# Kernel tuning notes

Hardware: AMD Instinct MI355X
Metric: run time of the kernel (lower is better)

## Reference

```python
import jax, jax.numpy as jnp
import numpy as np

B, S, D = 8, 1024, 1024

def setup_inputs() -> dict:
    key = jax.random.key(0)
    k1, k2, k3, k4, k5 = jax.random.split(key, 5)
    head = jax.random.normal(k1, (B, S, D), dtype=jnp.float32)
    dep = jax.random.normal(k2, (B, S, D), dtype=jnp.float32)
    edge_U = jax.random.normal(k3, (D, D), dtype=jnp.float32) * (1.0 / np.sqrt(D))
    edge_W = jax.random.normal(k4, (1, 2 * D), dtype=jnp.float32) * (1.0 / np.sqrt(2 * D))
    edge_b = jax.random.normal(k5, (1,), dtype=jnp.float32)
    return {"head": head, "dep": dep, "edge_U": edge_U, "edge_W": edge_W, "edge_b": edge_b}

def reference(head, dep, edge_U, edge_W, edge_b):
    # t1[b,i,j] = head[b,i,:] @ edge_U @ dep[b,j,:]
    t1 = jnp.einsum('bid,dk,bjk->bij', head, edge_U, dep)
    # t2: original concatenates [head_i ; dep_j] for every (i,j) pair and applies
    # edge_W [1, 2D]. Algebraically t2[b,i,j] = head_i @ W[:D] + dep_j @ W[D:],
    # so we compute two [B,S] projections and broadcast-add (same math, no
    # O(B*S^2*2D) intermediate).
    d = head.shape[-1]
    w = edge_W[0]
    s_head = head @ w[:d]   # [B, S]
    s_dep = dep @ w[d:]     # [B, S]
    return t1 + s_head[:, :, None] + s_dep[:, None, :] + edge_b[0]
```

## Files before the change

### kernel.cpp

```cpp
#include <hip/hip_runtime.h>
#include <hip/hip_bf16.h>
#include <stdint.h>

#define D_DIM 1024
#define B_DIM 8
#define S_DIM 1024

typedef __bf16 bf16;
typedef __bf16 bf16x4 __attribute__((ext_vector_type(4)));
typedef __bf16 bf16x8 __attribute__((ext_vector_type(8)));
typedef float floatx4 __attribute__((ext_vector_type(4)));

__device__ __forceinline__ void async_copy16(const void* g, void* l) {
    __builtin_amdgcn_global_load_lds(
        (const __attribute__((address_space(1))) void*)g,
        (__attribute__((address_space(3))) void*)l, 16, 0, 0);
}

__global__ __launch_bounds__(256) void prep_kernel(
    const float* __restrict__ head, const float* __restrict__ dep,
    const float* __restrict__ U, const float* __restrict__ edge_W,
    bf16* __restrict__ head_b, bf16* __restrict__ dep_b,
    bf16* __restrict__ U_b,
    float* __restrict__ s_head, float* __restrict__ s_dep)
{
    int blk  = blockIdx.x;
    int wid  = threadIdx.x >> 6;
    int lane = threadIdx.x & 63;

    if (blk < 4096) {
        int row = blk * 4 + wid;

        const float* src;
        bf16* dst;
        const float* w;
        float* sout;
        if (row < B_DIM * S_DIM) {
            src  = head   + (size_t)row * D_DIM;
            dst  = head_b + (size_t)row * D_DIM;
            w    = edge_W;
            sout = s_head + row;
        } else {
            int r = row - B_DIM * S_DIM;
            src  = dep   + (size_t)r * D_DIM;
            dst  = dep_b + (size_t)r * D_DIM;
            w    = edge_W + D_DIM;
            sout = s_dep + r;
        }
        float d = 0.0f;
        #pragma unroll
        for (int it = 0; it < 4; ++it) {
            int idx = it * 64 + lane;
            float4 v  = ((const float4*)src)[idx];
            float4 wv = ((const float4*)w)[idx];
            bf16x4 o;
            o[0] = (bf16)v.x; o[1] = (bf16)v.y; o[2] = (bf16)v.z; o[3] = (bf16)v.w;
            ((bf16x4*)dst)[idx] = o;
            d += v.x * wv.x + v.y * wv.y + v.z * wv.z + v.w * wv.w;
        }
        #pragma unroll
        for (int off = 32; off > 0; off >>= 1)
            d += __shfl_down(d, off, 64);
        if (lane == 0) *sout = d;
    } else {
        int row = (blk - 4096) * 4 + wid;
        const float* src = U   + (size_t)row * D_DIM;
        bf16*        dst = U_b + (size_t)row * D_DIM;
        #pragma unroll
        for (int it = 0; it < 4; ++it) {
            int idx = it * 64 + lane;
            float4 v = ((const float4*)src)[idx];
            bf16x4 o;
            o[0] = (bf16)v.x; o[1] = (bf16)v.y; o[2] = (bf16)v.z; o[3] = (bf16)v.w;
            ((bf16x4*)dst)[idx] = o;
        }
    }
}

template <int EPI>
__global__ __launch_bounds__(512, 4) void gemm_bt_kernel(
    const bf16* __restrict__ A, const bf16* __restrict__ Bt,
    void* __restrict__ Cout,
    int N,
    long long sA, long long sB, long long sC,
    const float* __restrict__ s_row, const float* __restrict__ s_col,
    const float* __restrict__ bias)
{
    const int BK = 64;
    __shared__ bf16 As[128 * BK];
    __shared__ bf16 Bs[128 * BK];

    int tid  = threadIdx.x;
    int wid  = tid >> 6;
    int lane = tid & 63;
    int quad = lane >> 4;
    int l16  = lane & 15;
    int wr   = wid >> 2;
    int wc   = wid & 3;

    int nx  = gridDim.x, ny = gridDim.y;
    int lin = blockIdx.x + nx * (blockIdx.y + ny * blockIdx.z);
    int nwg = nx * ny * gridDim.z;
    int swz = (lin & 7) * (nwg >> 3) + (lin >> 3);
    int bx  = swz % nx;
    int rem = swz / nx;
    int by  = rem % ny;
    int bz  = rem / ny;

    int tile_m = by * 128;
    int tile_n = bx * 128;

    const bf16* Ab = A  + (size_t)bz * sA + (size_t)tile_m * D_DIM;
    const bf16* Bb = Bt + (size_t)bz * sB + (size_t)tile_n * D_DIM;

    floatx4 zero = {0.0f, 0.0f, 0.0f, 0.0f};
    floatx4 acc[4][2];
    #pragma unroll
    for (int i = 0; i < 4; ++i)
        #pragma unroll
        for (int j = 0; j < 2; ++j) acc[i][j] = zero;

    for (int k0 = 0; k0 < D_DIM; k0 += BK) {
        #pragma unroll
        for (int it = 0; it < 2; ++it) {
            int g  = wid * 128 + it * 64 + lane;
            int r  = g >> 3;
            int cg = (g & 7) ^ (r & 7);
            int ldsoff = (wid * 128 + it * 64) * 8;
            async_copy16(Ab + (size_t)r * D_DIM + k0 + cg * 8, &As[ldsoff]);
            async_copy16(Bb + (size_t)r * D_DIM + k0 + cg * 8, &Bs[ldsoff]);
        }
        __syncthreads();

        #pragma unroll
        for (int kk = 0; kk < BK; kk += 32) {
            bf16x8 a[4], b[2];
            #pragma unroll
            for (int mt = 0; mt < 4; ++mt) {
                int row  = wr * 64 + mt * 16 + l16;
                int slot = ((kk >> 3) + quad) ^ (row & 7);
                a[mt] = *(const bf16x8*)&As[row * BK + slot * 8];
            }
            #pragma unroll
            for (int nt = 0; nt < 2; ++nt) {
                int row  = wc * 32 + nt * 16 + l16;
                int slot = ((kk >> 3) + quad) ^ (row & 7);
                b[nt] = *(const bf16x8*)&Bs[row * BK + slot * 8];
            }
            #pragma unroll
            for (int mt = 0; mt < 4; ++mt)
                #pragma unroll
                for (int nt = 0; nt < 2; ++nt)
                    acc[mt][nt] = __builtin_amdgcn_mfma_f32_16x16x32_bf16(
                        a[mt], b[nt], acc[mt][nt], 0, 0, 0);
        }
        __syncthreads();
    }

    int row0 = tile_m + wr * 64;
    int col0 = tile_n + wc * 32;
    if (EPI == 0) {
        bf16* Cb = (bf16*)Cout + (size_t)bz * sC;
        #pragma unroll
        for (int mt = 0; mt < 4; ++mt)
            #pragma unroll
            for (int r = 0; r < 4; ++r) {
                int row = row0 + mt * 16 + quad * 4 + r;
                #pragma unroll
                for (int nt = 0; nt < 2; ++nt) {
                    int col = col0 + nt * 16 + l16;
                    Cb[(size_t)row * N + col] = (bf16)acc[mt][nt][r];
                }
            }
    } else {
        float* Cf = (float*)Cout + (size_t)bz * sC;
        float b0 = bias[0];
        const float* srow = s_row + (size_t)bz * S_DIM;
        const float* scol = s_col + (size_t)bz * S_DIM;
        #pragma unroll
        for (int mt = 0; mt < 4; ++mt)
            #pragma unroll
            for (int r = 0; r < 4; ++r) {
                int row = row0 + mt * 16 + quad * 4 + r;
                float sh = srow[row] + b0;
                #pragma unroll
                for (int nt = 0; nt < 2; ++nt) {
                    int col = col0 + nt * 16 + l16;
                    __builtin_nontemporal_store(acc[mt][nt][r] + sh + scol[col],
                                                &Cf[(size_t)row * N + col]);
                }
            }
    }
}

extern "C" void kernel_launch(void* const* d_in, const int* in_sizes, int n_in,
                              void* d_out, int out_size, void* d_ws, size_t ws_size,
                              hipStream_t stream) {
    const float* head   = (const float*)d_in[0];
    const float* dep    = (const float*)d_in[1];
    const float* edge_U = (const float*)d_in[2];
    const float* edge_W = (const float*)d_in[3];
    const float* edge_b = (const float*)d_in[4];
    float* out = (float*)d_out;

    char* ws = (char*)d_ws;
    const size_t nBSD = (size_t)B_DIM * S_DIM * D_DIM;

    bf16*  head_b = (bf16*)ws;  ws += nBSD * sizeof(bf16);
    bf16*  dep_b  = (bf16*)ws;  ws += nBSD * sizeof(bf16);
    bf16*  U_b    = (bf16*)ws;  ws += (size_t)D_DIM * D_DIM * sizeof(bf16);
    bf16*  tmpD   = (bf16*)ws;  ws += nBSD * sizeof(bf16);
    float* s_head = (float*)ws; ws += (size_t)B_DIM * S_DIM * sizeof(float);
    float* s_dep  = (float*)ws; ws += (size_t)B_DIM * S_DIM * sizeof(float);

    prep_kernel<<<4096 + 256, 256, 0, stream>>>(
        head, dep, edge_U, edge_W, head_b, dep_b, U_b, s_head, s_dep);

    gemm_bt_kernel<0><<<dim3(D_DIM / 128, (B_DIM * S_DIM) / 128, 1), 512, 0, stream>>>(
        dep_b, U_b, tmpD, D_DIM,
        0, 0, 0, nullptr, nullptr, nullptr);

    gemm_bt_kernel<1><<<dim3(S_DIM / 128, S_DIM / 128, B_DIM), 512, 0, stream>>>(
        head_b, tmpD, out, S_DIM,
        (long long)S_DIM * D_DIM, (long long)S_DIM * D_DIM,
        (long long)S_DIM * S_DIM,
        s_head, s_dep, edge_b);
}
```

Before: 156.5 us.

## Double-buffer LDS K-slabs and enlarge GEMM tile to 256x128

Reworks the bf16 GEMM kernel so it prefetches the next K-slab into a second LDS buffer while MFMAs run on the current one, using explicit vmcnt waits and raw barriers. The M tile grows from 128 to 256, giving each wave 8x2 accumulators for more reuse of the B fragments. MFMA blocks are wrapped in s_setprio. The aim is to hide global-to-LDS latency and cut per-FLOP load traffic. The cost is more LDS and more registers (launch bounds drop to 2 blocks), and half as many workgroups, which lowers occupancy and parallelism across CUs.

```diff
diff --git a/kernel.cpp b/kernel.cpp
--- a/kernel.cpp
+++ b/kernel.cpp
@@ -77,8 +77,29 @@
     }
 }
 
+__device__ __forceinline__ void stage_slab(
+    const bf16* __restrict__ Ab, const bf16* __restrict__ Bb,
+    bf16* As, bf16* Bs, int k0, int wid, int lane)
+{
+    #pragma unroll
+    for (int it = 0; it < 4; ++it) {
+        int g  = wid * 256 + it * 64 + lane;
+        int r  = g >> 3;
+        int cg = (g & 7) ^ (r & 7);
+        int ldsoff = (wid * 256 + it * 64) * 8;
+        async_copy16(Ab + (size_t)r * D_DIM + k0 + cg * 8, &As[ldsoff]);
+        if (it < 2) {
+            int gb  = wid * 128 + it * 64 + lane;
+            int rb  = gb >> 3;
+            int cgb = (gb & 7) ^ (rb & 7);
+            int ldsoffb = (wid * 128 + it * 64) * 8;
+            async_copy16(Bb + (size_t)rb * D_DIM + k0 + cgb * 8, &Bs[ldsoffb]);
+        }
+    }
+}
+
 template <int EPI>
-__global__ __launch_bounds__(512, 4) void gemm_bt_kernel(
+__global__ __launch_bounds__(512, 2) void gemm_bt_kernel(
     const bf16* __restrict__ A, const bf16* __restrict__ Bt,
     void* __restrict__ Cout,
     int N,
@@ -86,9 +107,7 @@
     const float* __restrict__ s_row, const float* __restrict__ s_col,
     const float* __restrict__ bias)
 {
-    const int BK = 64;
-    __shared__ bf16 As[128 * BK];
-    __shared__ bf16 Bs[128 * BK];
+    __shared__ bf16 lds[2 * 24576];
 
     int tid  = threadIdx.x;
     int wid  = tid >> 6;
@@ -107,62 +126,69 @@
     int by  = rem % ny;
     int bz  = rem / ny;
 
-    int tile_m = by * 128;
+    int tile_m = by * 256;
     int tile_n = bx * 128;
 
     const bf16* Ab = A  + (size_t)bz * sA + (size_t)tile_m * D_DIM;
     const bf16* Bb = Bt + (size_t)bz * sB + (size_t)tile_n * D_DIM;
 
     floatx4 zero = {0.0f, 0.0f, 0.0f, 0.0f};
-    floatx4 acc[4][2];
+    floatx4 acc[8][2];
     #pragma unroll
-    for (int i = 0; i < 4; ++i)
+    for (int i = 0; i < 8; ++i)
         #pragma unroll
         for (int j = 0; j < 2; ++j) acc[i][j] = zero;
 
-    for (int k0 = 0; k0 < D_DIM; k0 += BK) {
-        #pragma unroll
-        for (int it = 0; it < 2; ++it) {
-            int g  = wid * 128 + it * 64 + lane;
-            int r  = g >> 3;
-            int cg = (g & 7) ^ (r & 7);
-            int ldsoff = (wid * 128 + it * 64) * 8;
-            async_copy16(Ab + (size_t)r * D_DIM + k0 + cg * 8, &As[ldsoff]);
-            async_copy16(Bb + (size_t)r * D_DIM + k0 + cg * 8, &Bs[ldsoff]);
-        }
-        __syncthreads();
-
-        #pragma unroll
-        for (int kk = 0; kk < BK; kk += 32) {
-            bf16x8 a[4], b[2];
-            #pragma unroll
-            for (int mt = 0; mt < 4; ++mt) {
-                int row  = wr * 64 + mt * 16 + l16;
+    const int NT = D_DIM / 64;
+
+    stage_slab(Ab, Bb, lds, lds + 16384, 0, wid, lane);
+
+    for (int t = 0; t < NT; ++t) {
+        bf16* As = lds + (t & 1) * 24576;
+        bf16* Bs = As + 16384;
+
+        if (t + 1 < NT) {
+            bf16* Asn = lds + ((t + 1) & 1) * 24576;
+            stage_slab(Ab, Bb, Asn, Asn + 16384, (t + 1) * 64, wid, lane);
+            asm volatile("s_waitcnt vmcnt(6)" ::: "memory");
+        } else {
+            asm volatile("s_waitcnt vmcnt(0)" ::: "memory");
+        }
+        asm volatile("s_barrier" ::: "memory");
+
+        #pragma unroll
+        for (int kk = 0; kk < 64; kk += 32) {
+            bf16x8 a[8], b[2];
+            #pragma unroll
+            for (int mt = 0; mt < 8; ++mt) {
+                int row  = wr * 128 + mt * 16 + l16;
                 int slot = ((kk >> 3) + quad) ^ (row & 7);
-                a[mt] = *(const bf16x8*)&As[row * BK + slot * 8];
+                a[mt] = *(const bf16x8*)&As[row * 64 + slot * 8];
             }
             #pragma unroll
             for (int nt = 0; nt < 2; ++nt) {
                 int row  = wc * 32 + nt * 16 + l16;
                 int slot = ((kk >> 3) + quad) ^ (row & 7);
-                b[nt] = *(const bf16x8*)&Bs[row * BK + slot * 8];
-            }
-            #pragma unroll
-            for (int mt = 0; mt < 4; ++mt)
+                b[nt] = *(const bf16x8*)&Bs[row * 64 + slot * 8];
+            }
+            __builtin_amdgcn_s_setprio(1);
+            #pragma unroll
+            for (int mt = 0; mt < 8; ++mt)
                 #pragma unroll
                 for (int nt = 0; nt < 2; ++nt)
                     acc[mt][nt] = __builtin_amdgcn_mfma_f32_16x16x32_bf16(
                         a[mt], b[nt], acc[mt][nt], 0, 0, 0);
-        }
-        __syncthreads();
-    }
-
-    int row0 = tile_m + wr * 64;
+            __builtin_amdgcn_s_setprio(0);
+            asm volatile("s_barrier" ::: "memory");
+        }
+    }
+
+    int row0 = tile_m + wr * 128;
     int col0 = tile_n + wc * 32;
     if (EPI == 0) {
         bf16* Cb = (bf16*)Cout + (size_t)bz * sC;
         #pragma unroll
-        for (int mt = 0; mt < 4; ++mt)
+        for (int mt = 0; mt < 8; ++mt)
             #pragma unroll
             for (int r = 0; r < 4; ++r) {
                 int row = row0 + mt * 16 + quad * 4 + r;
@@ -178,7 +204,7 @@
         const float* srow = s_row + (size_t)bz * S_DIM;
         const float* scol = s_col + (size_t)bz * S_DIM;
         #pragma unroll
-        for (int mt = 0; mt < 4; ++mt)
+        for (int mt = 0; mt < 8; ++mt)
             #pragma unroll
             for (int r = 0; r < 4; ++r) {
                 int row = row0 + mt * 16 + quad * 4 + r;
@@ -216,11 +242,11 @@
     prep_kernel<<<4096 + 256, 256, 0, stream>>>(
         head, dep, edge_U, edge_W, head_b, dep_b, U_b, s_head, s_dep);
 
-    gemm_bt_kernel<0><<<dim3(D_DIM / 128, (B_DIM * S_DIM) / 128, 1), 512, 0, stream>>>(
+    gemm_bt_kernel<0><<<dim3(D_DIM / 128, (B_DIM * S_DIM) / 256, 1), 512, 0, stream>>>(
         dep_b, U_b, tmpD, D_DIM,
         0, 0, 0, nullptr, nullptr, nullptr);
 
-    gemm_bt_kernel<1><<<dim3(S_DIM / 128, S_DIM / 128, B_DIM), 512, 0, stream>>>(
+    gemm_bt_kernel<1><<<dim3(S_DIM / 128, S_DIM / 256, B_DIM), 512, 0, stream>>>(
         head_b, tmpD, out, S_DIM,
         (long long)S_DIM * D_DIM, (long long)S_DIM * D_DIM,
         (long long)S_DIM * S_DIM,
```

Result: slower. 160.5 us (+2.5%).

## Enlarge GEMM tile to 256x128 with triple-buffered async LDS pipeline

Applied to the files above, without the earlier changes.

Reworks the bf16 GEMM kernel so each block computes a 256x128 tile, giving each wave 64x64 outputs. The K loop now uses a three-stage LDS ring with async global-to-LDS prefetch two tiles ahead, explicit vmcnt waits, raw s_barrier, and raised priority around the MFMA phases. The goal is to hide global load latency behind compute and to raise arithmetic intensity per LDS read. The cost is more LDS (about 144KB per block) and more accumulator registers, which lowers occupancy, and the hand-placed waitcnt and barriers must stay correct.

```diff
diff --git a/kernel.cpp b/kernel.cpp
--- a/kernel.cpp
+++ b/kernel.cpp
@@ -16,6 +16,9 @@
         (const __attribute__((address_space(1))) void*)g,
         (__attribute__((address_space(3))) void*)l, 16, 0, 0);
 }
+
+#define SBAR() do { asm volatile("s_barrier" ::: "memory"); \
+                    __builtin_amdgcn_sched_barrier(0); } while (0)
 
 __global__ __launch_bounds__(256) void prep_kernel(
     const float* __restrict__ head, const float* __restrict__ dep,
@@ -77,8 +80,62 @@
     }
 }
 
+__device__ __forceinline__ void stage_half(
+    const bf16* __restrict__ Ab, const bf16* __restrict__ Bb,
+    bf16* As, bf16* Bs, int k0, int wid, int lane, int half)
+{
+    #pragma unroll
+    for (int it = 0; it < 2; ++it) {
+        int ii = half * 2 + it;
+        int g  = wid * 256 + ii * 64 + lane;
+        int r  = g >> 3;
+        int cg = (g & 7) ^ (r & 7);
+        int ldsoff = (wid * 256 + ii * 64) * 8;
+        async_copy16(Ab + (size_t)r * D_DIM + k0 + cg * 8, &As[ldsoff]);
+    }
+    {
+        int gb  = wid * 128 + half * 64 + lane;
+        int rb  = gb >> 3;
+        int cgb = (gb & 7) ^ (rb & 7);
+        int ldsoffb = (wid * 128 + half * 64) * 8;
+        async_copy16(Bb + (size_t)rb * D_DIM + k0 + cgb * 8, &Bs[ldsoffb]);
+    }
+}
+
+__device__ __forceinline__ void phase_reads(
+    const bf16* As, const bf16* Bs, int kk,
+    int wr, int wc, int quad, int l16,
+    bf16x8 a[4], bf16x8 b[4])
+{
+    #pragma unroll
+    for (int mt = 0; mt < 4; ++mt) {
+        int row  = wr * 64 + mt * 16 + l16;
+        int slot = ((kk >> 3) + quad) ^ (row & 7);
+        a[mt] = *(const bf16x8*)&As[row * 64 + slot * 8];
+    }
+    #pragma unroll
+    for (int nt = 0; nt < 4; ++nt) {
+        int row  = wc * 64 + nt * 16 + l16;
+        int slot = ((kk >> 3) + quad) ^ (row & 7);
+        b[nt] = *(const bf16x8*)&Bs[row * 64 + slot * 8];
+    }
+}
+
+__device__ __forceinline__ void phase_fma(
+    const bf16x8 a[4], const bf16x8 b[4], floatx4 acc[4][4])
+{
+    __builtin_amdgcn_s_setprio(1);
+    #pragma unroll
+    for (int mt = 0; mt < 4; ++mt)
+        #pragma unroll
+        for (int nt = 0; nt < 4; ++nt)
+            acc[mt][nt] = __builtin_amdgcn_mfma_f32_16x16x32_bf16(
+                a[mt], b[nt], acc[mt][nt], 0, 0, 0);
+    __builtin_amdgcn_s_setprio(0);
+}
+
 template <int EPI>
-__global__ __launch_bounds__(512, 4) void gemm_bt_kernel(
+__global__ __launch_bounds__(512, 2) void gemm_bt_kernel(
     const bf16* __restrict__ A, const bf16* __restrict__ Bt,
     void* __restrict__ Cout,
     int N,
@@ -86,17 +143,15 @@
     const float* __restrict__ s_row, const float* __restrict__ s_col,
     const float* __restrict__ bias)
 {
-    const int BK = 64;
-    __shared__ bf16 As[128 * BK];
-    __shared__ bf16 Bs[128 * BK];
+    __shared__ bf16 lds[3 * 24576];
 
     int tid  = threadIdx.x;
     int wid  = tid >> 6;
     int lane = tid & 63;
     int quad = lane >> 4;
     int l16  = lane & 15;
-    int wr   = wid >> 2;
-    int wc   = wid & 3;
+    int wr   = wid & 3;
+    int wc   = wid >> 2;
 
     int nx  = gridDim.x, ny = gridDim.y;
     int lin = blockIdx.x + nx * (blockIdx.y + ny * blockIdx.z);
@@ -107,58 +162,55 @@
     int by  = rem % ny;
     int bz  = rem / ny;
 
-    int tile_m = by * 128;
+    int tile_m = by * 256;
     int tile_n = bx * 128;
 
     const bf16* Ab = A  + (size_t)bz * sA + (size_t)tile_m * D_DIM;
     const bf16* Bb = Bt + (size_t)bz * sB + (size_t)tile_n * D_DIM;
 
     floatx4 zero = {0.0f, 0.0f, 0.0f, 0.0f};
-    floatx4 acc[4][2];
+    floatx4 acc[4][4];
     #pragma unroll
     for (int i = 0; i < 4; ++i)
         #pragma unroll
-        for (int j = 0; j < 2; ++j) acc[i][j] = zero;
-
-    for (int k0 = 0; k0 < D_DIM; k0 += BK) {
-        #pragma unroll
-        for (int it = 0; it < 2; ++it) {
-            int g  = wid * 128 + it * 64 + lane;
-            int r  = g >> 3;
-            int cg = (g & 7) ^ (r & 7);
-            int ldsoff = (wid * 128 + it * 64) * 8;
-            async_copy16(Ab + (size_t)r * D_DIM + k0 + cg * 8, &As[ldsoff]);
-            async_copy16(Bb + (size_t)r * D_DIM + k0 + cg * 8, &Bs[ldsoff]);
-        }
-        __syncthreads();
-
-        #pragma unroll
-        for (int kk = 0; kk < BK; kk += 32) {
-            bf16x8 a[4], b[2];
-            #pragma unroll
-            for (int mt = 0; mt < 4; ++mt) {
-                int row  = wr * 64 + mt * 16 + l16;
-                int slot = ((kk >> 3) + quad) ^ (row & 7);
-                a[mt] = *(const bf16x8*)&As[row * BK + slot * 8];
-            }
-            #pragma unroll
-            for (int nt = 0; nt < 2; ++nt) {
-                int row  = wc * 32 + nt * 16 + l16;
-                int slot = ((kk >> 3) + quad) ^ (row & 7);
-                b[nt] = *(const bf16x8*)&Bs[row * BK + slot * 8];
-            }
-            #pragma unroll
-            for (int mt = 0; mt < 4; ++mt)
-                #pragma unroll
-                for (int nt = 0; nt < 2; ++nt)
-                    acc[mt][nt] = __builtin_amdgcn_mfma_f32_16x16x32_bf16(
-                        a[mt], b[nt], acc[mt][nt], 0, 0, 0);
-        }
-        __syncthreads();
+        for (int j = 0; j < 4; ++j) acc[i][j] = zero;
+
+    const int NT = D_DIM / 64;
+
+    stage_half(Ab, Bb, lds, lds + 16384, 0, wid, lane, 0);
+    stage_half(Ab, Bb, lds, lds + 16384, 0, wid, lane, 1);
+    stage_half(Ab, Bb, lds + 24576, lds + 24576 + 16384, 64, wid, lane, 0);
+    stage_half(Ab, Bb, lds + 24576, lds + 24576 + 16384, 64, wid, lane, 1);
+
+    for (int t = 0; t < NT; ++t) {
+        bf16* As  = lds + (t % 3) * 24576;
+        bf16* Bs  = As + 16384;
+        bf16* Asn = lds + ((t + 2) % 3) * 24576;
+        bf16* Bsn = Asn + 16384;
+        bool pf   = (t + 2 < NT);
+
+        if (t < NT - 1) asm volatile("s_waitcnt vmcnt(6)" ::: "memory");
+        else            asm volatile("s_waitcnt vmcnt(0)" ::: "memory");
+        SBAR();
+
+        {
+            bf16x8 a[4], b[4];
+            phase_reads(As, Bs, 0, wr, wc, quad, l16, a, b);
+            if (pf) stage_half(Ab, Bb, Asn, Bsn, (t + 2) * 64, wid, lane, 0);
+            SBAR();
+            phase_fma(a, b, acc);
+        }
+        {
+            bf16x8 a[4], b[4];
+            phase_reads(As, Bs, 32, wr, wc, quad, l16, a, b);
+            if (pf) stage_half(Ab, Bb, Asn, Bsn, (t + 2) * 64, wid, lane, 1);
+            SBAR();
+            phase_fma(a, b, acc);
+        }
     }
 
     int row0 = tile_m + wr * 64;
-    int col0 = tile_n + wc * 32;
+    int col0 = tile_n + wc * 64;
     if (EPI == 0) {
         bf16* Cb = (bf16*)Cout + (size_t)bz * sC;
         #pragma unroll
@@ -167,7 +219,7 @@
             for (int r = 0; r < 4; ++r) {
                 int row = row0 + mt * 16 + quad * 4 + r;
                 #pragma unroll
-                for (int nt = 0; nt < 2; ++nt) {
+                for (int nt = 0; nt < 4; ++nt) {
                     int col = col0 + nt * 16 + l16;
                     Cb[(size_t)row * N + col] = (bf16)acc[mt][nt][r];
                 }
@@ -184,7 +236,7 @@
                 int row = row0 + mt * 16 + quad * 4 + r;
                 float sh = srow[row] + b0;
                 #pragma unroll
-                for (int nt = 0; nt < 2; ++nt) {
+                for (int nt = 0; nt < 4; ++nt) {
                     int col = col0 + nt * 16 + l16;
                     __builtin_nontemporal_store(acc[mt][nt][r] + sh + scol[col],
                                                 &Cf[(size_t)row * N + col]);
@@ -216,11 +268,11 @@
     prep_kernel<<<4096 + 256, 256, 0, stream>>>(
         head, dep, edge_U, edge_W, head_b, dep_b, U_b, s_head, s_dep);
 
-    gemm_bt_kernel<0><<<dim3(D_DIM / 128, (B_DIM * S_DIM) / 128, 1), 512, 0, stream>>>(
+    gemm_bt_kernel<0><<<dim3(D_DIM / 128, (B_DIM * S_DIM) / 256, 1), 512, 0, stream>>>(
         dep_b, U_b, tmpD, D_DIM,
         0, 0, 0, nullptr, nullptr, nullptr);
 
-    gemm_bt_kernel<1><<<dim3(S_DIM / 128, S_DIM / 128, B_DIM), 512, 0, stream>>>(
+    gemm_bt_kernel<1><<<dim3(S_DIM / 128, S_DIM / 256, B_DIM), 512, 0, stream>>>(
         head_b, tmpD, out, S_DIM,
         (long long)S_DIM * D_DIM, (long long)S_DIM * D_DIM,
         (long long)S_DIM * S_DIM,
```

Result: no change. 155.7 us (-0.5%).

## Fuse fp32-to-bf16 conversion and projections into GEMM loads, drop prep kernel

Applied to the files above, without the earlier changes.

Removes the separate prep kernel and its bf16 copies of head, dep and U. Both GEMMs now load fp32 tiles into registers, convert them to bf16 while writing to LDS, and compute the edge_W row projections along the way. Loads are register-prefetched one K-step ahead and the MFMA blocks run under raised wave priority. This saves a full pass over the inputs and the intermediate writes. In exchange each GEMM reads fp32 (twice the bytes per tile) and the async global-to-LDS copies are replaced by synchronous register staging, with head and U re-converted by every tile that reads them.

```diff
diff --git a/kernel.cpp b/kernel.cpp
--- a/kernel.cpp
+++ b/kernel.cpp
@@ -11,84 +11,164 @@
 typedef __bf16 bf16x8 __attribute__((ext_vector_type(8)));
 typedef float floatx4 __attribute__((ext_vector_type(4)));
 
-__device__ __forceinline__ void async_copy16(const void* g, void* l) {
-    __builtin_amdgcn_global_load_lds(
-        (const __attribute__((address_space(1))) void*)g,
-        (__attribute__((address_space(3))) void*)l, 16, 0, 0);
+
+__device__ __forceinline__ bf16x4 cvt4(float4 v) {
+    bf16x4 o;
+    o[0] = (bf16)v.x; o[1] = (bf16)v.y; o[2] = (bf16)v.z; o[3] = (bf16)v.w;
+    return o;
 }
 
-__global__ __launch_bounds__(256) void prep_kernel(
-    const float* __restrict__ head, const float* __restrict__ dep,
-    const float* __restrict__ U, const float* __restrict__ edge_W,
-    bf16* __restrict__ head_b, bf16* __restrict__ dep_b,
-    bf16* __restrict__ U_b,
-    float* __restrict__ s_head, float* __restrict__ s_dep)
+
+
+__global__ __launch_bounds__(512) void gemm1_kernel(
+    const float* __restrict__ dep, const float* __restrict__ U,
+    const float* __restrict__ edge_W,
+    bf16* __restrict__ tmpD, float* __restrict__ s_dep)
 {
-    int blk  = blockIdx.x;
-    int wid  = threadIdx.x >> 6;
-    int lane = threadIdx.x & 63;
-
-    if (blk < 4096) {
-        int row = blk * 4 + wid;
-
-        const float* src;
-        bf16* dst;
-        const float* w;
-        float* sout;
-        if (row < B_DIM * S_DIM) {
-            src  = head   + (size_t)row * D_DIM;
-            dst  = head_b + (size_t)row * D_DIM;
-            w    = edge_W;
-            sout = s_head + row;
-        } else {
-            int r = row - B_DIM * S_DIM;
-            src  = dep   + (size_t)r * D_DIM;
-            dst  = dep_b + (size_t)r * D_DIM;
-            w    = edge_W + D_DIM;
-            sout = s_dep + r;
-        }
-        float d = 0.0f;
+    __shared__ bf16 As[128 * 64];
+    __shared__ bf16 Bs[128 * 64];
+
+    int tid  = threadIdx.x;
+    int wid  = tid >> 6;
+    int lane = tid & 63;
+    int quad = lane >> 4;
+    int l16  = lane & 15;
+    int wr   = wid >> 2;
+    int wc   = wid & 3;
+
+    int nx  = gridDim.x, ny = gridDim.y;
+    int lin = blockIdx.x + nx * blockIdx.y;
+    int nwg = nx * ny;
+    int swz = (lin & 7) * (nwg >> 3) + (lin >> 3);
+    int bx  = swz % nx;
+    int by  = swz / nx;
+
+    int tile_m = by * 128;
+    int tile_n = bx * 128;
+    const float* Ab = dep + (size_t)tile_m * D_DIM;
+    const float* Bb = U   + (size_t)tile_n * D_DIM;
+    const float* w2 = edge_W + D_DIM;
+    bool do_proj = (bx == 0);
+
+    int rA[4], cA[4];
+    #pragma unroll
+    for (int it = 0; it < 4; ++it) {
+        int idx = it * 512 + tid;
+        rA[it] = idx >> 4;
+        cA[it] = (idx & 15) * 4;
+    }
+
+    floatx4 zero = {0.0f, 0.0f, 0.0f, 0.0f};
+    floatx4 acc[4][2];
+    #pragma unroll
+    for (int i = 0; i < 4; ++i)
+        #pragma unroll
+        for (int j = 0; j < 2; ++j) acc[i][j] = zero;
+    float proj[4] = {0.f, 0.f, 0.f, 0.f};
+
+    float4 va[4], vb[4], vw[4];
+    #pragma unroll
+    for (int it = 0; it < 4; ++it) {
+        va[it] = *(const float4*)&Ab[(size_t)rA[it] * D_DIM + cA[it]];
+        vb[it] = *(const float4*)&Bb[(size_t)rA[it] * D_DIM + cA[it]];
+    }
+    if (do_proj) {
+        #pragma unroll
+        for (int it = 0; it < 4; ++it)
+            vw[it] = *(const float4*)&w2[cA[it]];
+    }
+
+    const int NT = D_DIM / 64;
+    for (int t = 0; t < NT; ++t) {
+        __syncthreads();
         #pragma unroll
         for (int it = 0; it < 4; ++it) {
-            int idx = it * 64 + lane;
-            float4 v  = ((const float4*)src)[idx];
-            float4 wv = ((const float4*)w)[idx];
-            bf16x4 o;
-            o[0] = (bf16)v.x; o[1] = (bf16)v.y; o[2] = (bf16)v.z; o[3] = (bf16)v.w;
-            ((bf16x4*)dst)[idx] = o;
-            d += v.x * wv.x + v.y * wv.y + v.z * wv.z + v.w * wv.w;
-        }
-        #pragma unroll
-        for (int off = 32; off > 0; off >>= 1)
-            d += __shfl_down(d, off, 64);
-        if (lane == 0) *sout = d;
-    } else {
-        int row = (blk - 4096) * 4 + wid;
-        const float* src = U   + (size_t)row * D_DIM;
-        bf16*        dst = U_b + (size_t)row * D_DIM;
+            int r   = rA[it];
+            int c16 = cA[it] >> 2;
+            int gg  = c16 >> 1, half = c16 & 1;
+            int off = r * 64 + ((gg ^ (r & 7)) * 8) + half * 4;
+            *(bf16x4*)&As[off] = cvt4(va[it]);
+            *(bf16x4*)&Bs[off] = cvt4(vb[it]);
+            if (do_proj)
+                proj[it] += va[it].x * vw[it].x + va[it].y * vw[it].y
+                          + va[it].z * vw[it].z + va[it].w * vw[it].w;
+        }
+        if (t + 1 < NT) {
+            int k0 = (t + 1) * 64;
+            #pragma unroll
+            for (int it = 0; it < 4; ++it) {
+                va[it] = *(const float4*)&Ab[(size_t)rA[it] * D_DIM + k0 + cA[it]];
+                vb[it] = *(const float4*)&Bb[(size_t)rA[it] * D_DIM + k0 + cA[it]];
+            }
+            if (do_proj) {
+                #pragma unroll
+                for (int it = 0; it < 4; ++it)
+                    vw[it] = *(const float4*)&w2[k0 + cA[it]];
+            }
+        }
+        __syncthreads();
+
+        #pragma unroll
+        for (int kk = 0; kk < 64; kk += 32) {
+            bf16x8 a[4], b[2];
+            #pragma unroll
+            for (int mt = 0; mt < 4; ++mt) {
+                int row  = wr * 64 + mt * 16 + l16;
+                int slot = ((kk >> 3) + quad) ^ (row & 7);
+                a[mt] = *(const bf16x8*)&As[row * 64 + slot * 8];
+            }
+            #pragma unroll
+            for (int nt = 0; nt < 2; ++nt) {
+                int row  = wc * 32 + nt * 16 + l16;
+                int slot = ((kk >> 3) + quad) ^ (row & 7);
+                b[nt] = *(const bf16x8*)&Bs[row * 64 + slot * 8];
+            }
+            __builtin_amdgcn_s_setprio(1);
+            #pragma unroll
+            for (int mt = 0; mt < 4; ++mt)
+                #pragma unroll
+                for (int nt = 0; nt < 2; ++nt)
+                    acc[mt][nt] = __builtin_amdgcn_mfma_f32_16x16x32_bf16(
+                        a[mt], b[nt], acc[mt][nt], 0, 0, 0);
+            __builtin_amdgcn_s_setprio(0);
+        }
+    }
+
+    if (do_proj) {
         #pragma unroll
         for (int it = 0; it < 4; ++it) {
-            int idx = it * 64 + lane;
-            float4 v = ((const float4*)src)[idx];
-            bf16x4 o;
-            o[0] = (bf16)v.x; o[1] = (bf16)v.y; o[2] = (bf16)v.z; o[3] = (bf16)v.w;
-            ((bf16x4*)dst)[idx] = o;
-        }
-    }
+            float v = proj[it];
+            v += __shfl_xor(v, 1, 16);
+            v += __shfl_xor(v, 2, 16);
+            v += __shfl_xor(v, 4, 16);
+            v += __shfl_xor(v, 8, 16);
+            if ((tid & 15) == 0) s_dep[tile_m + rA[it]] = v;
+        }
+    }
+
+    int row0 = tile_m + wr * 64;
+    int col0 = tile_n + wc * 32;
+    #pragma unroll
+    for (int mt = 0; mt < 4; ++mt)
+        #pragma unroll
+        for (int r = 0; r < 4; ++r) {
+            int row = row0 + mt * 16 + quad * 4 + r;
+            #pragma unroll
+            for (int nt = 0; nt < 2; ++nt) {
+                int col = col0 + nt * 16 + l16;
+                tmpD[(size_t)row * D_DIM + col] = (bf16)acc[mt][nt][r];
+            }
+        }
 }
 
-template <int EPI>
-__global__ __launch_bounds__(512, 4) void gemm_bt_kernel(
-    const bf16* __restrict__ A, const bf16* __restrict__ Bt,
-    void* __restrict__ Cout,
-    int N,
-    long long sA, long long sB, long long sC,
-    const float* __restrict__ s_row, const float* __restrict__ s_col,
-    const float* __restrict__ bias)
+__global__ __launch_bounds__(512) void gemm2_kernel(
+    const float* __restrict__ head, const bf16* __restrict__ tmpD,
+    const float* __restrict__ edge_W, const float* __restrict__ s_dep,
+    const float* __restrict__ edge_b, float* __restrict__ out)
 {
-    const int BK = 64;
-    __shared__ bf16 As[128 * BK];
-    __shared__ bf16 Bs[128 * BK];
+    __shared__ bf16 As[128 * 64];
+    __shared__ bf16 Bs[128 * 64];
+    __shared__ float smrow[128];
 
     int tid  = threadIdx.x;
     int wid  = tid >> 6;
@@ -109,9 +189,24 @@
 
     int tile_m = by * 128;
     int tile_n = bx * 128;
-
-    const bf16* Ab = A  + (size_t)bz * sA + (size_t)tile_m * D_DIM;
-    const bf16* Bb = Bt + (size_t)bz * sB + (size_t)tile_n * D_DIM;
+    const float* Ab = head + (size_t)bz * S_DIM * D_DIM + (size_t)tile_m * D_DIM;
+    const bf16*  Bb = tmpD + (size_t)bz * S_DIM * D_DIM + (size_t)tile_n * D_DIM;
+    const float* w1 = edge_W;
+
+    int rA[4], cA[4];
+    #pragma unroll
+    for (int it = 0; it < 4; ++it) {
+        int idx = it * 512 + tid;
+        rA[it] = idx >> 4;
+        cA[it] = (idx & 15) * 4;
+    }
+    int rB[2], gB[2];
+    #pragma unroll
+    for (int jt = 0; jt < 2; ++jt) {
+        int idx = jt * 512 + tid;
+        rB[jt] = idx >> 3;
+        gB[jt] = idx & 7;
+    }
 
     floatx4 zero = {0.0f, 0.0f, 0.0f, 0.0f};
     floatx4 acc[4][2];
@@ -119,78 +214,107 @@
     for (int i = 0; i < 4; ++i)
         #pragma unroll
         for (int j = 0; j < 2; ++j) acc[i][j] = zero;
-
-    for (int k0 = 0; k0 < D_DIM; k0 += BK) {
-        #pragma unroll
-        for (int it = 0; it < 2; ++it) {
-            int g  = wid * 128 + it * 64 + lane;
-            int r  = g >> 3;
-            int cg = (g & 7) ^ (r & 7);
-            int ldsoff = (wid * 128 + it * 64) * 8;
-            async_copy16(Ab + (size_t)r * D_DIM + k0 + cg * 8, &As[ldsoff]);
-            async_copy16(Bb + (size_t)r * D_DIM + k0 + cg * 8, &Bs[ldsoff]);
-        }
+    float proj[4] = {0.f, 0.f, 0.f, 0.f};
+
+    float4 va[4], vw[4];
+    bf16x8 pb[2];
+    #pragma unroll
+    for (int it = 0; it < 4; ++it) {
+        va[it] = *(const float4*)&Ab[(size_t)rA[it] * D_DIM + cA[it]];
+        vw[it] = *(const float4*)&w1[cA[it]];
+    }
+    #pragma unroll
+    for (int jt = 0; jt < 2; ++jt)
+        pb[jt] = *(const bf16x8*)&Bb[(size_t)rB[jt] * D_DIM + gB[jt] * 8];
+
+    const int NT = D_DIM / 64;
+    for (int t = 0; t < NT; ++t) {
         __syncthreads();
-
-        #pragma unroll
-        for (int kk = 0; kk < BK; kk += 32) {
+        #pragma unroll
+        for (int it = 0; it < 4; ++it) {
+            int r   = rA[it];
+            int c16 = cA[it] >> 2;
+            int gg  = c16 >> 1, half = c16 & 1;
+            int off = r * 64 + ((gg ^ (r & 7)) * 8) + half * 4;
+            *(bf16x4*)&As[off] = cvt4(va[it]);
+            proj[it] += va[it].x * vw[it].x + va[it].y * vw[it].y
+                      + va[it].z * vw[it].z + va[it].w * vw[it].w;
+        }
+        #pragma unroll
+        for (int jt = 0; jt < 2; ++jt) {
+            int r = rB[jt];
+            int off = r * 64 + ((gB[jt] ^ (r & 7)) * 8);
+            *(bf16x8*)&Bs[off] = pb[jt];
+        }
+        if (t + 1 < NT) {
+            int k0 = (t + 1) * 64;
+            #pragma unroll
+            for (int it = 0; it < 4; ++it) {
+                va[it] = *(const float4*)&Ab[(size_t)rA[it] * D_DIM + k0 + cA[it]];
+                vw[it] = *(const float4*)&w1[k0 + cA[it]];
+            }
+            #pragma unroll
+            for (int jt = 0; jt < 2; ++jt)
+                pb[jt] = *(const bf16x8*)&Bb[(size_t)rB[jt] * D_DIM + k0 + gB[jt] * 8];
+        }
+        __syncthreads();
+
+        #pragma unroll
+        for (int kk = 0; kk < 64; kk += 32) {
             bf16x8 a[4], b[2];
             #pragma unroll
             for (int mt = 0; mt < 4; ++mt) {
                 int row  = wr * 64 + mt * 16 + l16;
                 int slot = ((kk >> 3) + quad) ^ (row & 7);
-                a[mt] = *(const bf16x8*)&As[row * BK + slot * 8];
+                a[mt] = *(const bf16x8*)&As[row * 64 + slot * 8];
             }
             #pragma unroll
             for (int nt = 0; nt < 2; ++nt) {
                 int row  = wc * 32 + nt * 16 + l16;
                 int slot = ((kk >> 3) + quad) ^ (row & 7);
-                b[nt] = *(const bf16x8*)&Bs[row * BK + slot * 8];
-            }
+                b[nt] = *(const bf16x8*)&Bs[row * 64 + slot * 8];
+            }
+            __builtin_amdgcn_s_setprio(1);
             #pragma unroll
             for (int mt = 0; mt < 4; ++mt)
                 #pragma unroll
                 for (int nt = 0; nt < 2; ++nt)
                     acc[mt][nt] = __builtin_amdgcn_mfma_f32_16x16x32_bf16(
                         a[mt], b[nt], acc[mt][nt], 0, 0, 0);
-        }
-        __syncthreads();
-    }
-
-    int row0 = tile_m + wr * 64;
-    int col0 = tile_n + wc * 32;
-    if (EPI == 0) {
-        bf16* Cb = (bf16*)Cout + (size_t)bz * sC;
-        #pragma unroll
-        for (int mt = 0; mt < 4; ++mt)
-            #pragma unroll
-            for (int r = 0; r < 4; ++r) {
-                int row = row0 + mt * 16 + quad * 4 + r;
-                #pragma unroll
-                for (int nt = 0; nt < 2; ++nt) {
-                    int col = col0 + nt * 16 + l16;
-                    Cb[(size_t)row * N + col] = (bf16)acc[mt][nt][r];
-                }
-            }
-    } else {
-        float* Cf = (float*)Cout + (size_t)bz * sC;
-        float b0 = bias[0];
-        const float* srow = s_row + (size_t)bz * S_DIM;
-        const float* scol = s_col + (size_t)bz * S_DIM;
-        #pragma unroll
-        for (int mt = 0; mt < 4; ++mt)
-            #pragma unroll
-            for (int r = 0; r < 4; ++r) {
-                int row = row0 + mt * 16 + quad * 4 + r;
-                float sh = srow[row] + b0;
-                #pragma unroll
-                for (int nt = 0; nt < 2; ++nt) {
-                    int col = col0 + nt * 16 + l16;
-                    __builtin_nontemporal_store(acc[mt][nt][r] + sh + scol[col],
-                                                &Cf[(size_t)row * N + col]);
-                }
-            }
-    }
+            __builtin_amdgcn_s_setprio(0);
+        }
+    }
+
+    #pragma unroll
+    for (int it = 0; it < 4; ++it) {
+        float v = proj[it];
+        v += __shfl_xor(v, 1, 16);
+        v += __shfl_xor(v, 2, 16);
+        v += __shfl_xor(v, 4, 16);
+        v += __shfl_xor(v, 8, 16);
+        if ((tid & 15) == 0) smrow[rA[it]] = v;
+    }
+    __syncthreads();
+
+    float b0 = edge_b[0];
+    const float* scol = s_dep + (size_t)bz * S_DIM;
+    float* Cf = out + (size_t)bz * S_DIM * S_DIM;
+    int rloc0 = wr * 64;
+    int col0  = tile_n + wc * 32;
+    #pragma unroll
+    for (int mt = 0; mt < 4; ++mt)
+        #pragma unroll
+        for (int r = 0; r < 4; ++r) {
+            int rloc = rloc0 + mt * 16 + quad * 4 + r;
+            int row  = tile_m + rloc;
+            float sh = smrow[rloc] + b0;
+            #pragma unroll
+            for (int nt = 0; nt < 2; ++nt) {
+                int col = col0 + nt * 16 + l16;
+                __builtin_nontemporal_store(acc[mt][nt][r] + sh + scol[col],
+                                            &Cf[(size_t)row * S_DIM + col]);
+            }
+        }
 }
 
 extern "C" void kernel_launch(void* const* d_in, const int* in_sizes, int n_in,
@@ -206,23 +330,12 @@
     char* ws = (char*)d_ws;
     const size_t nBSD = (size_t)B_DIM * S_DIM * D_DIM;
 
-    bf16*  head_b = (bf16*)ws;  ws += nBSD * sizeof(bf16);
-    bf16*  dep_b  = (bf16*)ws;  ws += nBSD * sizeof(bf16);
-    bf16*  U_b    = (bf16*)ws;  ws += (size_t)D_DIM * D_DIM * sizeof(bf16);
-    bf16*  tmpD   = (bf16*)ws;  ws += nBSD * sizeof(bf16);
-    float* s_head = (float*)ws; ws += (size_t)B_DIM * S_DIM * sizeof(float);
-    float* s_dep  = (float*)ws; ws += (size_t)B_DIM * S_DIM * sizeof(float);
-
-    prep_kernel<<<4096 + 256, 256, 0, stream>>>(
-        head, dep, edge_U, edge_W, head_b, dep_b, U_b, s_head, s_dep);
-
-    gemm_bt_kernel<0><<<dim3(D_DIM / 128, (B_DIM * S_DIM) / 128, 1), 512, 0, stream>>>(
-        dep_b, U_b, tmpD, D_DIM,
-        0, 0, 0, nullptr, nullptr, nullptr);
-
-    gemm_bt_kernel<1><<<dim3(S_DIM / 128, S_DIM / 128, B_DIM), 512, 0, stream>>>(
-        head_b, tmpD, out, S_DIM,
-        (long long)S_DIM * D_DIM, (long long)S_DIM * D_DIM,
-        (long long)S_DIM * S_DIM,
-        s_head, s_dep, edge_b);
+    bf16*  tmpD  = (bf16*)ws;  ws += nBSD * sizeof(bf16);
+    float* s_dep = (float*)ws; ws += (size_t)B_DIM * S_DIM * sizeof(float);
+
+    gemm1_kernel<<<dim3(D_DIM / 128, (B_DIM * S_DIM) / 128, 1), 512, 0, stream>>>(
+        dep, edge_U, edge_W, tmpD, s_dep);
+
+    gemm2_kernel<<<dim3(S_DIM / 128, S_DIM / 128, B_DIM), 512, 0, stream>>>(
+        head, tmpD, edge_W, s_dep, edge_b, out);
 }
```

Result: slower. 195.5 us (+24.9%).
